# Kernel tuning notes

Measured on AMD Instinct MI355X. Metric: run time of the kernel, lower is better.

## Reference

```python
import jax, jax.numpy as jnp
import numpy as np

N = 100000
E = 1600000
D = 128


def _sage_conv(x, src, dst, W_l, W_r, b):
    # PyG SAGEConv (aggr='mean', project=False, root_weight=True):
    #   out = lin_l(mean_{j in N(i)} x_j) + lin_r(x_i), bias lives in lin_l.
    msg = x[src]                                            # [E, D] gather
    s = jax.ops.segment_sum(msg, dst, num_segments=N)       # [N, D]
    cnt = jax.ops.segment_sum(jnp.ones((src.shape[0],), x.dtype), dst, num_segments=N)
    mean = s / jnp.maximum(cnt, 1.0)[:, None]               # mean aggregation
    return mean @ W_l.T + x @ W_r.T + b


def setup_inputs() -> dict:
    key = jax.random.key(0)
    ks = jax.random.split(key, 8)
    x = jax.random.normal(ks[0], (N, D), dtype=jnp.float32)
    edge_index = jax.random.randint(ks[1], (2, E), 0, N, dtype=jnp.int64)
    scale = 1.0 / np.sqrt(D)
    params = {}
    for i, k in enumerate(ks[2:8]):
        pass
    W_l1 = jax.random.uniform(ks[2], (D, D), jnp.float32, -scale, scale)
    W_r1 = jax.random.uniform(ks[3], (D, D), jnp.float32, -scale, scale)
    W_l2 = jax.random.uniform(ks[4], (D, D), jnp.float32, -scale, scale)
    W_r2 = jax.random.uniform(ks[5], (D, D), jnp.float32, -scale, scale)
    W_l3 = jax.random.uniform(ks[6], (D, D), jnp.float32, -scale, scale)
    W_r3 = jax.random.uniform(ks[7], (D, D), jnp.float32, -scale, scale)
    b1 = jnp.zeros((D,), jnp.float32)
    b2 = jnp.zeros((D,), jnp.float32)
    b3 = jnp.zeros((D,), jnp.float32)
    return {"x": x, "edge_index": edge_index,
            "W_l1": W_l1, "W_r1": W_r1, "b1": b1,
            "W_l2": W_l2, "W_r2": W_r2, "b2": b2,
            "W_l3": W_l3, "W_r3": W_r3, "b3": b3}


def reference(x, edge_index, W_l1, W_r1, b1, W_l2, W_r2, b2, W_l3, W_r3, b3):
    src, dst = edge_index[0], edge_index[1]
    h = jax.nn.relu(_sage_conv(x, src, dst, W_l1, W_r1, b1))
    h = jax.nn.relu(_sage_conv(h, src, dst, W_l2, W_r2, b2))
    h = _sage_conv(h, src, dst, W_l3, W_r3, b3)
    return h
```

## Files before the change

### kernel.cpp

```cpp
#include <hip/hip_runtime.h>


typedef __bf16 bf16x8 __attribute__((ext_vector_type(8)));
typedef float  f32x4  __attribute__((ext_vector_type(4)));

#define DFEAT 128
#define PAD 64
#define PITCH 136
#define BSH 7
#define BNODES 128
#define CAP 3072
#define CHUNK 8192
#define NBMAX 1024

__device__ __forceinline__ unsigned int pack_bf16x2(float2 v) {
    unsigned int lo = (unsigned int)__builtin_bit_cast(unsigned short, (__bf16)v.x);
    unsigned int hi = (unsigned int)__builtin_bit_cast(unsigned short, (__bf16)v.y);
    return lo | (hi << 16);
}

struct WPtrs  { const float* s[6]; };
struct WBPtrs { unsigned int* d[6]; };

__global__ __launch_bounds__(256) void k_pass1(const int* __restrict__ src,
                                               const int* __restrict__ dst, int E,
                                               int nb, int eblk,
                                               int* __restrict__ galloc,
                                               unsigned int* __restrict__ binned,
                                               const float* __restrict__ x,
                                               uint2* __restrict__ xb4,
                                               int xw4, int xblk,
                                               WPtrs ws, WBPtrs wd) {
    __shared__ int cnt[NBMAX], cnt2[NBMAX], sbase[NBMAX];
    int b = blockIdx.x;
    int t = threadIdx.x;
    if (b < eblk) {
        for (int i = t; i < nb; i += 256) { cnt[i] = 0; cnt2[i] = 0; }
        __syncthreads();
        int e0 = b * CHUNK;
        int dcache[32];
#pragma unroll
        for (int j = 0; j < 32; ++j) {
            int e = e0 + j * 256 + t;
            int d = (e < E) ? dst[e] : -1;
            dcache[j] = d;
            if (d >= 0) atomicAdd(&cnt[d >> BSH], 1);
        }
        __syncthreads();
        for (int i = t; i < nb; i += 256) {
            int c = cnt[i];
            sbase[i] = (c > 0) ? atomicAdd(&galloc[i << 4], c) : 0;
        }
        __syncthreads();
        int r[32];
#pragma unroll
        for (int j = 0; j < 32; ++j) {
            int d = dcache[j];
            r[j] = (d >= 0) ? atomicAdd(&cnt2[d >> BSH], 1) : 0;
        }
#pragma unroll
        for (int j = 0; j < 32; ++j) {
            int d = dcache[j];
            if (d >= 0) {
                int e = e0 + j * 256 + t;
                unsigned s = (unsigned)src[e];
                int bk = d >> BSH;
                int idx = sbase[bk] + r[j];
                if (idx < CAP)
                    binned[(size_t)bk * CAP + idx] =
                        s | ((unsigned)(d & (BNODES - 1)) << 20);
            }
        }
    } else if (b < eblk + xblk) {
        int i = (b - eblk) * 256 + t;
        if (i < xw4) {
            float4 v = ((const float4*)x)[i];
            uint2 o;
            o.x = pack_bf16x2(make_float2(v.x, v.y));
            o.y = pack_bf16x2(make_float2(v.z, v.w));
            xb4[i] = o;
        }
    } else {
        int r = b - eblk - xblk;
        int which = r >> 5;
        int i = (r & 31) * 256 + t;
        wd.d[which][i] = pack_bf16x2(((const float2*)ws.s[which])[i]);
    }
}

__global__ __launch_bounds__(256) void k_pass2(const int* __restrict__ galloc,
                                               const unsigned int* __restrict__ binned,
                                               int* __restrict__ csr,
                                               int* __restrict__ deg, int N) {
    __shared__ int lcnt[BNODES];
    __shared__ __align__(16) int lcsr[BNODES * PAD];
    int b = blockIdx.x, t = threadIdx.x;
    if (t < BNODES) lcnt[t] = 0;
    int4 zfill = make_int4(N, N, N, N);
    int4* l4 = (int4*)lcsr;
    for (int i = t; i < BNODES * PAD / 4; i += 256) l4[i] = zfill;
    __syncthreads();
    int ne = galloc[b << 4];
    if (ne > CAP) ne = CAP;
    for (int i = t; i < ne; i += 256) {
        unsigned v = binned[(size_t)b * CAP + i];
        int nl = (int)(v >> 20);
        int s  = (int)(v & 0xFFFFFu);
        int r = atomicAdd(&lcnt[nl], 1);
        if (r < PAD) lcsr[(nl << 6) + r] = s;
    }
    __syncthreads();
    int node0 = b << BSH;
    int NL = N - node0;
    if (NL > BNODES) NL = BNODES;
    const uint4* ls4 = (const uint4*)lcsr;
    uint4* cs4 = (uint4*)(csr + ((size_t)node0 << 6));
    int n4 = NL * 16;
    for (int i = t; i < n4; i += 256) cs4[i] = ls4[i];
    if (t < NL) deg[node0 + t] = min(lcnt[t], PAD);
}

__global__ __launch_bounds__(256, 4) void k_layer(const __bf16* __restrict__ h,
                                               const int* __restrict__ deg,
                                               const int* __restrict__ csr,
                                               const __bf16* __restrict__ Wl,
                                               const __bf16* __restrict__ Wr,
                                               const float* __restrict__ bias,
                                               __bf16* __restrict__ outb,
                                               float* __restrict__ outf,
                                               int relu) {
    __shared__ __bf16 sm[2][16][PITCH];
    int tid  = threadIdx.x;
    int wave = tid >> 6;
    int lane = tid & 63;
    int g = lane >> 4;
    int c = lane & 15;
    int t0 = blockIdx.x * 16;
    int node = t0 + (wave << 2) + g;
    int row = (wave << 2) + g;

    const uint4* hp4 = (const uint4*)h;

    *(uint4*)&sm[1][row][c * 8] = hp4[(size_t)node * 16 + c];

    int d = deg[node];
    if (d > PAD) d = PAD;
    float acc[8];
#pragma unroll
    for (int j = 0; j < 8; ++j) acc[j] = 0.0f;

    for (int s0 = 0; s0 < d; s0 += 16) {
        int myedge = csr[(node << 6) + s0 + c];
#pragma unroll
        for (int hb = 0; hb < 2; ++hb) {
            uint4 u[8];
#pragma unroll
            for (int kk = 0; kk < 8; ++kk) {
                int s = __shfl(myedge, (g << 4) + hb * 8 + kk, 64);
                u[kk] = hp4[(size_t)s * 16 + c];
            }
#pragma unroll
            for (int kk = 0; kk < 8; ++kk) {
                unsigned int w0 = u[kk].x, w1 = u[kk].y, w2 = u[kk].z, w3 = u[kk].w;
                acc[0] += __uint_as_float(w0 << 16);
                acc[1] += __uint_as_float(w0 & 0xffff0000u);
                acc[2] += __uint_as_float(w1 << 16);
                acc[3] += __uint_as_float(w1 & 0xffff0000u);
                acc[4] += __uint_as_float(w2 << 16);
                acc[5] += __uint_as_float(w2 & 0xffff0000u);
                acc[6] += __uint_as_float(w3 << 16);
                acc[7] += __uint_as_float(w3 & 0xffff0000u);
            }
        }
    }
    float iv = (d > 0) ? 1.0f / (float)d : 0.0f;
    uint4 o;
    o.x = pack_bf16x2(make_float2(acc[0] * iv, acc[1] * iv));
    o.y = pack_bf16x2(make_float2(acc[2] * iv, acc[3] * iv));
    o.z = pack_bf16x2(make_float2(acc[4] * iv, acc[5] * iv));
    o.w = pack_bf16x2(make_float2(acc[6] * iv, acc[7] * iv));
    *(uint4*)&sm[0][row][c * 8] = o;

    int m = lane & 15;
    int q = lane >> 4;
    bf16x8 wf[2][4][2];
#pragma unroll
    for (int half = 0; half < 2; ++half) {
        const __bf16* W = half ? Wr : Wl;
#pragma unroll
        for (int kk = 0; kk < 4; ++kk) {
            int k0 = kk * 32 + q * 8;
#pragma unroll
            for (int jt = 0; jt < 2; ++jt) {
                int j = wave * 32 + jt * 16 + m;
                wf[half][kk][jt] = *(const bf16x8*)(W + (size_t)j * DFEAT + k0);
            }
        }
    }

    __syncthreads();

    f32x4 accj[2];
    accj[0] = (f32x4){0.f, 0.f, 0.f, 0.f};
    accj[1] = (f32x4){0.f, 0.f, 0.f, 0.f};

#pragma unroll
    for (int half = 0; half < 2; ++half) {
#pragma unroll
        for (int kk = 0; kk < 4; ++kk) {
            int k0 = kk * 32 + q * 8;
            bf16x8 a = *(const bf16x8*)&sm[half][m][k0];
#pragma unroll
            for (int jt = 0; jt < 2; ++jt) {
                accj[jt] = __builtin_amdgcn_mfma_f32_16x16x32_bf16(a, wf[half][kk][jt],
                                                                   accj[jt], 0, 0, 0);
            }
        }
    }

#pragma unroll
    for (int jt = 0; jt < 2; ++jt) {
        int j = wave * 32 + jt * 16 + m;
        float bv = bias[j];
#pragma unroll
        for (int r = 0; r < 4; ++r) {
            float v = accj[jt][r] + bv;
            if (relu) v = fmaxf(v, 0.0f);
            size_t idx = (size_t)(t0 + q * 4 + r) * DFEAT + j;
            if (outb) outb[idx] = (__bf16)v;
            else      outf[idx] = v;
        }
    }
}

extern "C" void kernel_launch(void* const* d_in, const int* in_sizes, int n_in,
                              void* d_out, int out_size, void* d_ws, size_t ws_size,
                              hipStream_t stream) {
    const int N = in_sizes[0] / DFEAT;
    const int E = in_sizes[1] / 2;

    const float* x   = (const float*)d_in[0];
    const int*   ei  = (const int*)d_in[1];
    const int*   src = ei;
    const int*   dst = ei + E;
    const float* b1  = (const float*)d_in[4];
    const float* b2  = (const float*)d_in[7];
    const float* b3  = (const float*)d_in[10];
    float* out = (float*)d_out;

    char* base = (char*)d_ws;
    size_t off = 0;
    auto alloc = [&](size_t nbytes) -> void* {
        off = (off + 255) & ~(size_t)255;
        void* p = base + off;
        off += nbytes;
        return p;
    };
    const int NB = (N + BNODES - 1) >> BSH;
    const size_t ROW_B = (size_t)DFEAT * 2;
    const size_t FEAT_B = (size_t)(N + 1) * ROW_B;
    int*    deg    = (int*)alloc((size_t)N * 4);
    int*    csr    = (int*)alloc((size_t)N * PAD * 4);
    int*    galloc = (int*)alloc((size_t)NB * 64);
    __bf16* xb  = (__bf16*)alloc(FEAT_B);
    __bf16* h1b = (__bf16*)alloc(FEAT_B);
    __bf16* h2b = (__bf16*)alloc(FEAT_B);
    __bf16* Wb[6];
    for (int i = 0; i < 6; ++i) Wb[i] = (__bf16*)alloc((size_t)DFEAT * DFEAT * 2);
    (void)ws_size;
    unsigned int* binned = (unsigned int*)h2b;

    const int EB1  = (E + CHUNK - 1) / CHUNK;
    const int XW4  = N * DFEAT / 4;
    const int XBLK = (XW4 + 255) / 256;
    const int TILE_B = N / 16;

    WPtrs  wsrc = {{(const float*)d_in[2], (const float*)d_in[3],
                    (const float*)d_in[5], (const float*)d_in[6],
                    (const float*)d_in[8], (const float*)d_in[9]}};
    WBPtrs wdst = {{(unsigned int*)Wb[0], (unsigned int*)Wb[1],
                    (unsigned int*)Wb[2], (unsigned int*)Wb[3],
                    (unsigned int*)Wb[4], (unsigned int*)Wb[5]}};

    hipMemsetAsync(galloc, 0, (size_t)NB * 64, stream);
    hipMemsetAsync(xb  + (size_t)N * DFEAT, 0, ROW_B, stream);
    hipMemsetAsync(h1b + (size_t)N * DFEAT, 0, ROW_B, stream);
    hipMemsetAsync(h2b + (size_t)N * DFEAT, 0, ROW_B, stream);

    k_pass1<<<EB1 + XBLK + 6 * 32, 256, 0, stream>>>(src, dst, E, NB, EB1, galloc,
                                                     binned, x, (uint2*)xb,
                                                     XW4, XBLK, wsrc, wdst);
    k_pass2<<<NB, 256, 0, stream>>>(galloc, binned, csr, deg, N);

    k_layer<<<TILE_B, 256, 0, stream>>>(xb,  deg, csr, Wb[0], Wb[1], b1, h1b, nullptr, 1);
    k_layer<<<TILE_B, 256, 0, stream>>>(h1b, deg, csr, Wb[2], Wb[3], b2, h2b, nullptr, 1);
    k_layer<<<TILE_B, 256, 0, stream>>>(h2b, deg, csr, Wb[4], Wb[5], b3, nullptr, out, 0);
}
```

Baseline: 433.7 us.

## Switch features to chunked column-major layout with 128-node fused gather+MFMA tiles

Feature buffers are stored as 8 chunks of 16 bf16 columns per node, so each gather pass reads a compact 32-byte slice per neighbor and the working set per chunk is smaller, which should help L2 hit rate. Each block now handles 128 nodes. It aggregates chunk by chunk into a global scratch buffer, then runs MFMA with the weights as the A operand and features as B, with 8 node tiles per wave. This removes the LDS staging and the per-16-node weight reload, but it adds a round trip of the mean through global memory and 8 separate csr re-reads per node. The binned scratch moves to the output buffer, and the sentinel-row zeroing moves into pass1.

Measured after the change: 843.3 us. +94.4%, slower.

```diff
diff --git a/kernel.cpp b/kernel.cpp
--- a/kernel.cpp
+++ b/kernel.cpp
@@ -6,7 +6,7 @@
 
 #define DFEAT 128
 #define PAD 64
-#define PITCH 136
+#define NTILE 128
 #define BSH 7
 #define BNODES 128
 #define CAP 3072
@@ -21,6 +21,7 @@
 
 struct WPtrs  { const float* s[6]; };
 struct WBPtrs { unsigned int* d[6]; };
+struct ZPtrs  { __bf16* d[3]; };
 
 __global__ __launch_bounds__(256) void k_pass1(const int* __restrict__ src,
                                                const int* __restrict__ dst, int E,
@@ -28,9 +29,10 @@
                                                int* __restrict__ galloc,
                                                unsigned int* __restrict__ binned,
                                                const float* __restrict__ x,
-                                               uint2* __restrict__ xb4,
-                                               int xw4, int xblk,
-                                               WPtrs ws, WBPtrs wd) {
+                                               __bf16* __restrict__ xb,
+                                               int xw, int xblk,
+                                               WPtrs ws, WBPtrs wd, ZPtrs zs,
+                                               int N, int cstride) {
     __shared__ int cnt[NBMAX], cnt2[NBMAX], sbase[NBMAX];
     int b = blockIdx.x;
     int t = threadIdx.x;
@@ -73,18 +75,32 @@
         }
     } else if (b < eblk + xblk) {
         int i = (b - eblk) * 256 + t;
-        if (i < xw4) {
-            float4 v = ((const float4*)x)[i];
-            uint2 o;
-            o.x = pack_bf16x2(make_float2(v.x, v.y));
-            o.y = pack_bf16x2(make_float2(v.z, v.w));
-            xb4[i] = o;
-        }
-    } else {
+        if (i < xw) {
+            int n = i >> 4;
+            int s = i & 15;
+            const float4* xp = (const float4*)(x + (size_t)n * DFEAT + s * 8);
+            float4 v0 = xp[0], v1 = xp[1];
+            uint4 o;
+            o.x = pack_bf16x2(make_float2(v0.x, v0.y));
+            o.y = pack_bf16x2(make_float2(v0.z, v0.w));
+            o.z = pack_bf16x2(make_float2(v1.x, v1.y));
+            o.w = pack_bf16x2(make_float2(v1.z, v1.w));
+            *(uint4*)(xb + (size_t)(s >> 1) * cstride + (size_t)n * 16 +
+                      (s & 1) * 8) = o;
+        }
+    } else if (b < eblk + xblk + 192) {
         int r = b - eblk - xblk;
         int which = r >> 5;
         int i = (r & 31) * 256 + t;
         wd.d[which][i] = pack_bf16x2(((const float2*)ws.s[which])[i]);
+    } else {
+        if (t < 48) {
+            int bi = t >> 4;
+            int r2 = t & 15;
+            int ch = r2 >> 1, hf = r2 & 1;
+            *(uint4*)(zs.d[bi] + (size_t)ch * cstride + (size_t)N * 16 +
+                      hf * 8) = make_uint4(0u, 0u, 0u, 0u);
+        }
     }
 }
 
@@ -120,115 +136,130 @@
     if (t < NL) deg[node0 + t] = min(lcnt[t], PAD);
 }
 
-__global__ __launch_bounds__(256, 4) void k_layer(const __bf16* __restrict__ h,
-                                               const int* __restrict__ deg,
-                                               const int* __restrict__ csr,
-                                               const __bf16* __restrict__ Wl,
-                                               const __bf16* __restrict__ Wr,
-                                               const float* __restrict__ bias,
-                                               __bf16* __restrict__ outb,
-                                               float* __restrict__ outf,
-                                               int relu) {
-    __shared__ __bf16 sm[2][16][PITCH];
-    int tid  = threadIdx.x;
-    int wave = tid >> 6;
-    int lane = tid & 63;
-    int g = lane >> 4;
-    int c = lane & 15;
-    int t0 = blockIdx.x * 16;
-    int node = t0 + (wave << 2) + g;
-    int row = (wave << 2) + g;
-
-    const uint4* hp4 = (const uint4*)h;
-
-    *(uint4*)&sm[1][row][c * 8] = hp4[(size_t)node * 16 + c];
-
-    int d = deg[node];
-    if (d > PAD) d = PAD;
-    float acc[8];
-#pragma unroll
-    for (int j = 0; j < 8; ++j) acc[j] = 0.0f;
-
-    for (int s0 = 0; s0 < d; s0 += 16) {
-        int myedge = csr[(node << 6) + s0 + c];
-#pragma unroll
-        for (int hb = 0; hb < 2; ++hb) {
-            uint4 u[8];
-#pragma unroll
-            for (int kk = 0; kk < 8; ++kk) {
-                int s = __shfl(myedge, (g << 4) + hb * 8 + kk, 64);
-                u[kk] = hp4[(size_t)s * 16 + c];
+__global__ __launch_bounds__(256, 4) void k_fused(const __bf16* __restrict__ fb,
+                                                  const int* __restrict__ deg,
+                                                  const int* __restrict__ csr,
+                                                  __bf16* __restrict__ mb,
+                                                  const __bf16* __restrict__ Wl,
+                                                  const __bf16* __restrict__ Wr,
+                                                  const float* __restrict__ bias,
+                                                  __bf16* __restrict__ outb,
+                                                  float* __restrict__ outf,
+                                                  int relu, int N, int cstride) {
+    int tid = threadIdx.x;
+    int wv = tid >> 6;
+    int l = tid & 63;
+    int t0 = blockIdx.x * NTILE;
+
+    {
+        int n2 = l >> 1, p = l & 1;
+        int node = t0 + (wv << 5) + n2;
+        int d = (node < N) ? deg[node] : 0;
+        if (d > PAD) d = PAD;
+        float iv = d ? 1.0f / (float)d : 0.0f;
+        int nb = (d + 7) >> 3;
+        const uint4* csr4 = (const uint4*)csr;
+        size_t crow = (size_t)node * 16;
+
+#pragma unroll 1
+        for (int ch = 0; ch < 8; ++ch) {
+            const uint4* f4 = (const uint4*)(fb + (size_t)ch * cstride);
+            float acc[8];
+#pragma unroll
+            for (int j = 0; j < 8; ++j) acc[j] = 0.0f;
+            for (int it = 0; it < nb; ++it) {
+                uint4 ia = csr4[crow + it * 2];
+                uint4 ib = csr4[crow + it * 2 + 1];
+                uint4 u[8];
+                u[0] = f4[(size_t)(unsigned)ia.x * 2 + p];
+                u[1] = f4[(size_t)(unsigned)ia.y * 2 + p];
+                u[2] = f4[(size_t)(unsigned)ia.z * 2 + p];
+                u[3] = f4[(size_t)(unsigned)ia.w * 2 + p];
+                u[4] = f4[(size_t)(unsigned)ib.x * 2 + p];
+                u[5] = f4[(size_t)(unsigned)ib.y * 2 + p];
+                u[6] = f4[(size_t)(unsigned)ib.z * 2 + p];
+                u[7] = f4[(size_t)(unsigned)ib.w * 2 + p];
+#pragma unroll
+                for (int j = 0; j < 8; ++j) {
+                    acc[0] += __uint_as_float(u[j].x << 16);
+                    acc[1] += __uint_as_float(u[j].x & 0xffff0000u);
+                    acc[2] += __uint_as_float(u[j].y << 16);
+                    acc[3] += __uint_as_float(u[j].y & 0xffff0000u);
+                    acc[4] += __uint_as_float(u[j].z << 16);
+                    acc[5] += __uint_as_float(u[j].z & 0xffff0000u);
+                    acc[6] += __uint_as_float(u[j].w << 16);
+                    acc[7] += __uint_as_float(u[j].w & 0xffff0000u);
+                }
             }
-#pragma unroll
-            for (int kk = 0; kk < 8; ++kk) {
-                unsigned int w0 = u[kk].x, w1 = u[kk].y, w2 = u[kk].z, w3 = u[kk].w;
-                acc[0] += __uint_as_float(w0 << 16);
-                acc[1] += __uint_as_float(w0 & 0xffff0000u);
-                acc[2] += __uint_as_float(w1 << 16);
-                acc[3] += __uint_as_float(w1 & 0xffff0000u);
-                acc[4] += __uint_as_float(w2 << 16);
-                acc[5] += __uint_as_float(w2 & 0xffff0000u);
-                acc[6] += __uint_as_float(w3 << 16);
-                acc[7] += __uint_as_float(w3 & 0xffff0000u);
-            }
-        }
-    }
-    float iv = (d > 0) ? 1.0f / (float)d : 0.0f;
-    uint4 o;
-    o.x = pack_bf16x2(make_float2(acc[0] * iv, acc[1] * iv));
-    o.y = pack_bf16x2(make_float2(acc[2] * iv, acc[3] * iv));
-    o.z = pack_bf16x2(make_float2(acc[4] * iv, acc[5] * iv));
-    o.w = pack_bf16x2(make_float2(acc[6] * iv, acc[7] * iv));
-    *(uint4*)&sm[0][row][c * 8] = o;
-
-    int m = lane & 15;
-    int q = lane >> 4;
-    bf16x8 wf[2][4][2];
+            uint4 o;
+            o.x = pack_bf16x2(make_float2(acc[0] * iv, acc[1] * iv));
+            o.y = pack_bf16x2(make_float2(acc[2] * iv, acc[3] * iv));
+            o.z = pack_bf16x2(make_float2(acc[4] * iv, acc[5] * iv));
+            o.w = pack_bf16x2(make_float2(acc[6] * iv, acc[7] * iv));
+            *(uint4*)(mb + (size_t)ch * cstride + (size_t)node * 16 + p * 8) = o;
+        }
+    }
+
+    __syncthreads();
+
+    int q = l >> 4, c = l & 15;
+    f32x4 acc2[8][2];
+#pragma unroll
+    for (int nt = 0; nt < 8; ++nt) {
+        acc2[nt][0] = (f32x4){0.f, 0.f, 0.f, 0.f};
+        acc2[nt][1] = (f32x4){0.f, 0.f, 0.f, 0.f};
+    }
+
 #pragma unroll
     for (int half = 0; half < 2; ++half) {
         const __bf16* W = half ? Wr : Wl;
+        const __bf16* F = half ? fb : mb;
 #pragma unroll
         for (int kk = 0; kk < 4; ++kk) {
-            int k0 = kk * 32 + q * 8;
+            int koff = kk * 32 + q * 8;
+            bf16x8 a0 = *(const bf16x8*)(W + (size_t)(wv * 32 + c) * DFEAT + koff);
+            bf16x8 a1 = *(const bf16x8*)(W + (size_t)(wv * 32 + 16 + c) * DFEAT + koff);
+            const __bf16* Fc = F + (size_t)(kk * 2 + (q >> 1)) * cstride + (q & 1) * 8;
+#pragma unroll
+            for (int nt = 0; nt < 8; ++nt) {
+                int bn = t0 + nt * 16 + c;
+                bf16x8 bfr = *(const bf16x8*)(Fc + (size_t)bn * 16);
+                acc2[nt][0] = __builtin_amdgcn_mfma_f32_16x16x32_bf16(a0, bfr,
+                                                                      acc2[nt][0], 0, 0, 0);
+                acc2[nt][1] = __builtin_amdgcn_mfma_f32_16x16x32_bf16(a1, bfr,
+                                                                      acc2[nt][1], 0, 0, 0);
+            }
+        }
+    }
+
+    float4 bv0 = *(const float4*)(bias + wv * 32 + q * 4);
+    float4 bv1 = *(const float4*)(bias + wv * 32 + 16 + q * 4);
+#pragma unroll
+    for (int nt = 0; nt < 8; ++nt) {
+        int bn = t0 + nt * 16 + c;
+        if (bn < N) {
 #pragma unroll
             for (int jt = 0; jt < 2; ++jt) {
-                int j = wave * 32 + jt * 16 + m;
-                wf[half][kk][jt] = *(const bf16x8*)(W + (size_t)j * DFEAT + k0);
+                float4 bv = jt ? bv1 : bv0;
+                float v0 = acc2[nt][jt][0] + bv.x;
+                float v1 = acc2[nt][jt][1] + bv.y;
+                float v2 = acc2[nt][jt][2] + bv.z;
+                float v3 = acc2[nt][jt][3] + bv.w;
+                if (relu) {
+                    v0 = fmaxf(v0, 0.f); v1 = fmaxf(v1, 0.f);
+                    v2 = fmaxf(v2, 0.f); v3 = fmaxf(v3, 0.f);
+                }
+                if (outb) {
+                    uint2 pk;
+                    pk.x = pack_bf16x2(make_float2(v0, v1));
+                    pk.y = pack_bf16x2(make_float2(v2, v3));
+                    *(uint2*)(outb + (size_t)(wv * 2 + jt) * cstride +
+                              (size_t)bn * 16 + q * 4) = pk;
+                } else {
+                    *(float4*)(outf + (size_t)bn * DFEAT + wv * 32 + jt * 16 +
+                               q * 4) = make_float4(v0, v1, v2, v3);
+                }
             }
-        }
-    }
-
-    __syncthreads();
-
-    f32x4 accj[2];
-    accj[0] = (f32x4){0.f, 0.f, 0.f, 0.f};
-    accj[1] = (f32x4){0.f, 0.f, 0.f, 0.f};
-
-#pragma unroll
-    for (int half = 0; half < 2; ++half) {
-#pragma unroll
-        for (int kk = 0; kk < 4; ++kk) {
-            int k0 = kk * 32 + q * 8;
-            bf16x8 a = *(const bf16x8*)&sm[half][m][k0];
-#pragma unroll
-            for (int jt = 0; jt < 2; ++jt) {
-                accj[jt] = __builtin_amdgcn_mfma_f32_16x16x32_bf16(a, wf[half][kk][jt],
-                                                                   accj[jt], 0, 0, 0);
-            }
-        }
-    }
-
-#pragma unroll
-    for (int jt = 0; jt < 2; ++jt) {
-        int j = wave * 32 + jt * 16 + m;
-        float bv = bias[j];
-#pragma unroll
-        for (int r = 0; r < 4; ++r) {
-            float v = accj[jt][r] + bv;
-            if (relu) v = fmaxf(v, 0.0f);
-            size_t idx = (size_t)(t0 + q * 4 + r) * DFEAT + j;
-            if (outb) outb[idx] = (__bf16)v;
-            else      outf[idx] = v;
         }
     }
 }
@@ -257,8 +288,11 @@
         return p;
     };
     const int NB = (N + BNODES - 1) >> BSH;
-    const size_t ROW_B = (size_t)DFEAT * 2;
-    const size_t FEAT_B = (size_t)(N + 1) * ROW_B;
+    const int NT = (N + NTILE - 1) / NTILE;
+    const int CNROWS = NT * NTILE;
+    const int CSTRIDE = CNROWS * 16;
+    const size_t FEAT_B = (size_t)8 * CSTRIDE * 2;
+
     int*    deg    = (int*)alloc((size_t)N * 4);
     int*    csr    = (int*)alloc((size_t)N * PAD * 4);
     int*    galloc = (int*)alloc((size_t)NB * 64);
@@ -268,31 +302,30 @@
     __bf16* Wb[6];
     for (int i = 0; i < 6; ++i) Wb[i] = (__bf16*)alloc((size_t)DFEAT * DFEAT * 2);
     (void)ws_size;
-    unsigned int* binned = (unsigned int*)h2b;
+    unsigned int* binned = (unsigned int*)d_out;
 
     const int EB1  = (E + CHUNK - 1) / CHUNK;
-    const int XW4  = N * DFEAT / 4;
-    const int XBLK = (XW4 + 255) / 256;
-    const int TILE_B = N / 16;
-
+    const int XW   = N * 16;
+    const int XBLK = (XW + 255) / 256;
     WPtrs  wsrc = {{(const float*)d_in[2], (const float*)d_in[3],
                     (const float*)d_in[5], (const float*)d_in[6],
                     (const float*)d_in[8], (const float*)d_in[9]}};
     WBPtrs wdst = {{(unsigned int*)Wb[0], (unsigned int*)Wb[1],
                     (unsigned int*)Wb[2], (unsigned int*)Wb[3],
                     (unsigned int*)Wb[4], (unsigned int*)Wb[5]}};
+    ZPtrs  zs   = {{xb, h1b, h2b}};
 
     hipMemsetAsync(galloc, 0, (size_t)NB * 64, stream);
-    hipMemsetAsync(xb  + (size_t)N * DFEAT, 0, ROW_B, stream);
-    hipMemsetAsync(h1b + (size_t)N * DFEAT, 0, ROW_B, stream);
-    hipMemsetAsync(h2b + (size_t)N * DFEAT, 0, ROW_B, stream);
-
-    k_pass1<<<EB1 + XBLK + 6 * 32, 256, 0, stream>>>(src, dst, E, NB, EB1, galloc,
-                                                     binned, x, (uint2*)xb,
-                                                     XW4, XBLK, wsrc, wdst);
+    k_pass1<<<EB1 + XBLK + 192 + 1, 256, 0, stream>>>(src, dst, E, NB, EB1,
+                                                      galloc, binned, x, xb,
+                                                      XW, XBLK, wsrc, wdst, zs,
+                                                      N, CSTRIDE);
     k_pass2<<<NB, 256, 0, stream>>>(galloc, binned, csr, deg, N);
 
-    k_layer<<<TILE_B, 256, 0, stream>>>(xb,  deg, csr, Wb[0], Wb[1], b1, h1b, nullptr, 1);
-    k_layer<<<TILE_B, 256, 0, stream>>>(h1b, deg, csr, Wb[2], Wb[3], b2, h2b, nullptr, 1);
-    k_layer<<<TILE_B, 256, 0, stream>>>(h2b, deg, csr, Wb[4], Wb[5], b3, nullptr, out, 0);
-}
+    k_fused<<<NT, 256, 0, stream>>>(xb,  deg, csr, h2b, Wb[0], Wb[1], b1,
+                                    h1b, nullptr, 1, N, CSTRIDE);
+    k_fused<<<NT, 256, 0, stream>>>(h1b, deg, csr, xb,  Wb[2], Wb[3], b2,
+                                    h2b, nullptr, 1, N, CSTRIDE);
+    k_fused<<<NT, 256, 0, stream>>>(h2b, deg, csr, h1b, Wb[4], Wb[5], b3,
+                                    nullptr, out, 0, N, CSTRIDE);
+}
```
